# Optimization experiments

Measured on AMD Instinct MI355X. Metric: run time of the kernel, lower is better.

## Reference

```python
import jax, jax.numpy as jnp
import numpy as np

NI, NF = 100000, 2000
E, EF = 800000, 200000
DN, DE = 16, 8
NH, EH = 64, 8
NL = 11

def setup_inputs() -> dict:
    key = jax.random.key(0)
    ks = jax.random.split(key, 24)
    g = lambda k, shp, fan: jax.random.normal(k, shp, jnp.float32) / np.float32(np.sqrt(fan))
    inp = {
        'instruction_feats': jax.random.normal(ks[0], (NI, DN), jnp.float32),
        'final_feats': jax.random.normal(ks[1], (NF, DN), jnp.float32),
        'instruction_edge_feats': jax.random.normal(ks[2], (E, DE), jnp.float32),
        'to_final_edge_feats': jax.random.normal(ks[3], (EF, DE), jnp.float32),
        'prev_src': jax.random.randint(ks[4], (E,), 0, NI, jnp.int32),
        'prev_dst': jax.random.randint(ks[5], (E,), 0, NI, jnp.int32),
        'tf_src': jax.random.randint(ks[6], (EF,), 0, NI, jnp.int32),
        'tf_dst': jax.random.randint(ks[7], (EF,), 0, NF, jnp.int32),
        'W_it': g(ks[8], (DN, NH), DN), 'b_it': jnp.zeros((NH,), jnp.float32),
        'W_ft': g(ks[9], (DN, NH), DN), 'b_ft': jnp.zeros((NH,), jnp.float32),
        'W_ep': g(ks[10], (DE, EH), DE), 'b_ep': jnp.zeros((EH,), jnp.float32),
        'W_es': g(ks[11], (DE, EH), DE), 'b_es': jnp.zeros((EH,), jnp.float32),
        'W_ef': g(ks[12], (DE, EH), DE), 'b_ef': jnp.zeros((EH,), jnp.float32),
        'Wg_prev': g(ks[13], (NL, NH + EH, NH), NH + EH), 'bg_prev': jnp.zeros((NL, NH), jnp.float32),
        'Wg_succ': g(ks[14], (NL, NH + EH, NH), NH + EH), 'bg_succ': jnp.zeros((NL, NH), jnp.float32),
        'Wg_tf': g(ks[15], (NL, NH + EH, NH), NH + EH), 'bg_tf': jnp.zeros((NL, NH), jnp.float32),
        'Wr1': g(ks[16], (NH, NH), NH), 'br1': jnp.zeros((NH,), jnp.float32),
        'Wr2': g(ks[17], (NH, NH), NH), 'br2': jnp.zeros((NH,), jnp.float32),
        'Wr3': g(ks[18], (NH, 1), NH), 'br3': jnp.zeros((1,), jnp.float32),
    }
    return inp

def _mean_agg(src_feats, src_idx, dst_idx, edge_feats, W, b, n_dst):
    # gather-concat-dense per edge, then scatter-mean onto destinations
    msg = jnp.concatenate([src_feats[src_idx], edge_feats], axis=1) @ W + b  # [E, NH]
    s = jax.ops.segment_sum(msg, dst_idx, num_segments=n_dst)
    cnt = jax.ops.segment_sum(jnp.ones((msg.shape[0], 1), msg.dtype), dst_idx, num_segments=n_dst)
    return s / jnp.maximum(cnt, 1.0)  # zero-in-degree nodes get 0 (DGL mean semantics)

def reference(instruction_feats, final_feats, instruction_edge_feats, to_final_edge_feats,
              prev_src, prev_dst, tf_src, tf_dst,
              W_it, b_it, W_ft, b_ft, W_ep, b_ep, W_es, b_es, W_ef, b_ef,
              Wg_prev, bg_prev, Wg_succ, bg_succ, Wg_tf, bg_tf,
              Wr1, br1, Wr2, br2, Wr3, br3):
    elu = jax.nn.elu
    ni = instruction_feats.shape[0]
    nf = final_feats.shape[0]
    inst = elu(instruction_feats @ W_it + b_it)
    fin = elu(final_feats @ W_ft + b_ft)
    e_prev = elu(instruction_edge_feats @ W_ep + b_ep)
    e_succ = elu(instruction_edge_feats @ W_es + b_es)
    e_tf = elu(to_final_edge_feats @ W_ef + b_ef)
    succ_src, succ_dst = prev_dst, prev_src  # 'succ' is the reverse edge set
    for l in range(Wg_prev.shape[0]):
        o_p = _mean_agg(inst, prev_src, prev_dst, e_prev, Wg_prev[l], bg_prev[l], ni)
        o_s = _mean_agg(inst, succ_src, succ_dst, e_succ, Wg_succ[l], bg_succ[l], ni)
        o_f = _mean_agg(inst, tf_src, tf_dst, e_tf, Wg_tf[l], bg_tf[l], nf)
        inst = elu(inst + 0.5 * (o_p + o_s))
        fin = elu(fin + o_f)
    fin = elu(fin @ Wr1 + br1)
    fin = elu(fin @ Wr2 + br2)
    return jnp.squeeze(fin @ Wr3 + br3, axis=1)
```

## Files before the change

### kernel.cpp

```cpp
#include <hip/hip_runtime.h>
#include <math.h>

#define NI 100000
#define NF 2000
#define NE 800000
#define NEF 200000
#define DN 16
#define NL 11
#define NT (2 * NI + NF)
#define KX 160
#define NBI 782
#define NBF 125
#define WTN (64 * 168)

typedef short bf16x8 __attribute__((ext_vector_type(8)));
typedef float f32x4 __attribute__((ext_vector_type(4)));

__device__ __forceinline__ float elu1(float x) { return x > 0.f ? x : expm1f(x); }

__device__ __forceinline__ unsigned short f2bf(float f) {
    unsigned x = __float_as_uint(f);
    return (unsigned short)((x + 0x7fffu + ((x >> 16) & 1u)) >> 16);
}
__device__ __forceinline__ float bf2f(unsigned short u) {
    return __uint_as_float(((unsigned)u) << 16);
}

__global__ __launch_bounds__(256) void k_count(const int* __restrict__ prev_src,
                                               const int* __restrict__ prev_dst,
                                               const int* __restrict__ tf_dst,
                                               int* cnt) {
    int i = blockIdx.x * blockDim.x + threadIdx.x;
    if (i < NE) {
        atomicAdd(&cnt[prev_dst[i]], 1);
        atomicAdd(&cnt[NI + prev_src[i]], 1);
    }
    if (i < NEF) atomicAdd(&cnt[2 * NI + tf_dst[i]], 1);
}

__global__ __launch_bounds__(256) void k_scan1(const int* __restrict__ cnt, int n,
                                               int* __restrict__ rp, int* __restrict__ bsum) {
    __shared__ int s[256];
    int t = threadIdx.x, b = blockIdx.x, i = b * 256 + t;
    int v = (i < n) ? cnt[i] : 0;
    s[t] = v; __syncthreads();
    for (int o = 1; o < 256; o <<= 1) {
        int x = (t >= o) ? s[t - o] : 0;
        __syncthreads();
        s[t] += x;
        __syncthreads();
    }
    if (i < n) rp[i + 1] = s[t];
    if (t == 255) bsum[b] = s[255];
}

__global__ __launch_bounds__(1024) void k_scan2(int* __restrict__ bsum, int nb) {
    __shared__ int s[1024];
    int t = threadIdx.x;
    int v = (t < nb) ? bsum[t] : 0;
    s[t] = v; __syncthreads();
    for (int o = 1; o < 1024; o <<= 1) {
        int x = (t >= o) ? s[t - o] : 0;
        __syncthreads();
        s[t] += x;
        __syncthreads();
    }
    if (t < nb) bsum[t] = s[t] - v;
}

__global__ __launch_bounds__(256) void k_scan3(int* __restrict__ rp, const int* __restrict__ bsum, int n) {
    int i = blockIdx.x * blockDim.x + threadIdx.x;
    if (i < n) rp[i + 1] += bsum[i >> 8];
    if (i == 0) rp[0] = 0;
}

__global__ __launch_bounds__(256) void k_prep_w(const float* __restrict__ Wg_prev,
                                                const float* __restrict__ Wg_succ,
                                                unsigned short* __restrict__ wcat) {
    int idx = blockIdx.x * blockDim.x + threadIdx.x;
    if (idx >= NL * WTN) return;
    int l = idx / WTN;
    int r = idx - l * WTN;
    int n = r / 168, k = r - n * 168;
    float v = 0.f;
    if (k < 72)       v = 0.5f * Wg_prev[(size_t)l * 72 * 64 + k * 64 + n];
    else if (k < 144) v = 0.5f * Wg_succ[(size_t)l * 72 * 64 + (k - 72) * 64 + n];
    wcat[idx] = f2bf(v);
}

__global__ __launch_bounds__(256) void k_scatter(const int* __restrict__ prev_src,
                                                 const int* __restrict__ prev_dst,
                                                 const int* __restrict__ tf_src,
                                                 const int* __restrict__ tf_dst,
                                                 const float* __restrict__ xe,
                                                 const float* __restrict__ xef,
                                                 const int* __restrict__ rp,
                                                 int* fill,
                                                 int* colP, int* colS, int* colF,
                                                 float* __restrict__ ePbuf,
                                                 float* __restrict__ eSbuf,
                                                 float* __restrict__ eFbuf,
                                                 const float* __restrict__ Wep, const float* __restrict__ bep,
                                                 const float* __restrict__ Wes, const float* __restrict__ bes,
                                                 const float* __restrict__ Wef, const float* __restrict__ bef) {
    int i = blockIdx.x * blockDim.x + threadIdx.x;
    if (i < NE) {
        int s = prev_src[i], d = prev_dst[i];
        float4 x0 = ((const float4*)xe)[(size_t)i * 2];
        float4 x1 = ((const float4*)xe)[(size_t)i * 2 + 1];
        float x[8] = {x0.x, x0.y, x0.z, x0.w, x1.x, x1.y, x1.z, x1.w};
        float eP[8], eS[8];
#pragma unroll
        for (int j = 0; j < 8; j++) {
            float vp = bep[j], vs = bes[j];
#pragma unroll
            for (int k = 0; k < 8; k++) { vp += x[k] * Wep[k * 8 + j]; vs += x[k] * Wes[k * 8 + j]; }
            eP[j] = elu1(vp); eS[j] = elu1(vs);
        }
        int tP = rp[d] + atomicAdd(&fill[d], 1);
        colP[tP] = s;
        ((float4*)ePbuf)[(size_t)tP * 2]     = make_float4(eP[0], eP[1], eP[2], eP[3]);
        ((float4*)ePbuf)[(size_t)tP * 2 + 1] = make_float4(eP[4], eP[5], eP[6], eP[7]);
        int tS = rp[NI + s] - NE + atomicAdd(&fill[NI + s], 1);
        colS[tS] = d;
        ((float4*)eSbuf)[(size_t)tS * 2]     = make_float4(eS[0], eS[1], eS[2], eS[3]);
        ((float4*)eSbuf)[(size_t)tS * 2 + 1] = make_float4(eS[4], eS[5], eS[6], eS[7]);
    }
    if (i < NEF) {
        int s = tf_src[i], d = tf_dst[i];
        float4 x0 = ((const float4*)xef)[(size_t)i * 2];
        float4 x1 = ((const float4*)xef)[(size_t)i * 2 + 1];
        float x[8] = {x0.x, x0.y, x0.z, x0.w, x1.x, x1.y, x1.z, x1.w};
        float eF[8];
#pragma unroll
        for (int j = 0; j < 8; j++) {
            float v = bef[j];
#pragma unroll
            for (int k = 0; k < 8; k++) v += x[k] * Wef[k * 8 + j];
            eF[j] = elu1(v);
        }
        int tF = rp[2 * NI + d] - 2 * NE + atomicAdd(&fill[2 * NI + d], 1);
        colF[tF] = s;
        ((float4*)eFbuf)[(size_t)tF * 2]     = make_float4(eF[0], eF[1], eF[2], eF[3]);
        ((float4*)eFbuf)[(size_t)tF * 2 + 1] = make_float4(eF[4], eF[5], eF[6], eF[7]);
    }
}

__global__ __launch_bounds__(256) void k_eagg2(const int* __restrict__ rp,
                                               const float* __restrict__ ePbuf,
                                               const float* __restrict__ eSbuf,
                                               const float* __restrict__ eFbuf,
                                               float* __restrict__ aggEp,
                                               float* __restrict__ aggEs,
                                               float* __restrict__ aggEf) {
    int idx = blockIdx.x * blockDim.x + threadIdx.x;
    if (idx >= NT) return;
    const float* buf; float* out; int s, e;
    if (idx < NF) {
        int n = idx;
        s = rp[2 * NI + n] - 2 * NE; e = rp[2 * NI + n + 1] - 2 * NE;
        buf = eFbuf; out = aggEf + (size_t)n * 8;
    } else if (idx < NF + NI) {
        int n = idx - NF;
        s = rp[n]; e = rp[n + 1];
        buf = ePbuf; out = aggEp + (size_t)n * 8;
    } else {
        int n = idx - NF - NI;
        s = rp[NI + n] - NE; e = rp[NI + n + 1] - NE;
        buf = eSbuf; out = aggEs + (size_t)n * 8;
    }
    float a0 = 0.f, a1 = 0.f, a2 = 0.f, a3 = 0.f, a4 = 0.f, a5 = 0.f, a6 = 0.f, a7 = 0.f;
    for (int t = s; t < e; ++t) {
        float4 v0 = ((const float4*)buf)[(size_t)t * 2];
        float4 v1 = ((const float4*)buf)[(size_t)t * 2 + 1];
        a0 += v0.x; a1 += v0.y; a2 += v0.z; a3 += v0.w;
        a4 += v1.x; a5 += v1.y; a6 += v1.z; a7 += v1.w;
    }
    ((float4*)out)[0] = make_float4(a0, a1, a2, a3);
    ((float4*)out)[1] = make_float4(a4, a5, a6, a7);
}

__global__ __launch_bounds__(256) void k_prep_x(const int* __restrict__ rpAll,
                                                const float* __restrict__ aggEp,
                                                const float* __restrict__ aggEs,
                                                unsigned short* __restrict__ X) {
    int i = blockIdx.x * blockDim.x + threadIdx.x;
    if (i >= NI) return;
    int cP = rpAll[i + 1] - rpAll[i];
    int cS = rpAll[NI + i + 1] - rpAll[NI + i];
    float invP = 1.f / (float)max(cP, 1);
    float invS = 1.f / (float)max(cS, 1);
    unsigned short* xr = X + (size_t)i * KX;
#pragma unroll
    for (int c = 0; c < 2; c++) {
        float4 ep = ((const float4*)(aggEp + (size_t)i * 8))[c];
        float4 es = ((const float4*)(aggEs + (size_t)i * 8))[c];
        ushort4 up; up.x = f2bf(ep.x * invP); up.y = f2bf(ep.y * invP);
                    up.z = f2bf(ep.z * invP); up.w = f2bf(ep.w * invP);
        ushort4 us; us.x = f2bf(es.x * invS); us.y = f2bf(es.y * invS);
                    us.z = f2bf(es.z * invS); us.w = f2bf(es.w * invS);
        ((ushort4*)(xr + 64))[c]  = up;
        ((ushort4*)(xr + 136))[c] = us;
    }
    ushort4 z; z.x = z.y = z.z = z.w = 0;
#pragma unroll
    for (int c = 0; c < 4; c++) ((ushort4*)(xr + 144))[c] = z;
}

__global__ __launch_bounds__(256) void k_node_embed(const float* __restrict__ xi,
                                                    const float* __restrict__ xf,
                                                    const float* __restrict__ Wit, const float* __restrict__ bit,
                                                    const float* __restrict__ Wft, const float* __restrict__ bft,
                                                    float* __restrict__ inst, unsigned short* __restrict__ inst_bf,
                                                    float* __restrict__ fin) {
    const int NPW = 16;
    int lane = threadIdx.x & 63;
    int wave = (blockIdx.x * blockDim.x + threadIdx.x) >> 6;
    int base = wave * NPW;
    float wi[DN], wf[DN];
#pragma unroll
    for (int k = 0; k < DN; k++) { wi[k] = Wit[k * 64 + lane]; wf[k] = Wft[k * 64 + lane]; }
    float bi = bit[lane], bf = bft[lane];
    for (int n = 0; n < NPW; n++) {
        int i = base + n;
        if (i < NI) {
            const float4* x4 = (const float4*)(xi + (size_t)i * DN);
            float4 xa = x4[0], xb = x4[1], xc = x4[2], xd = x4[3];
            float x[DN] = {xa.x, xa.y, xa.z, xa.w, xb.x, xb.y, xb.z, xb.w,
                           xc.x, xc.y, xc.z, xc.w, xd.x, xd.y, xd.z, xd.w};
            float acc = bi;
#pragma unroll
            for (int k = 0; k < DN; k++) acc += x[k] * wi[k];
            float v = elu1(acc);
            inst[(size_t)i * 64 + lane] = v;
            inst_bf[(size_t)i * 64 + lane] = f2bf(v);
        } else if (i < NI + NF) {
            int f = i - NI;
            const float4* x4 = (const float4*)(xf + (size_t)f * DN);
            float4 xa = x4[0], xb = x4[1], xc = x4[2], xd = x4[3];
            float x[DN] = {xa.x, xa.y, xa.z, xa.w, xb.x, xb.y, xb.z, xb.w,
                           xc.x, xc.y, xc.z, xc.w, xd.x, xd.y, xd.z, xd.w};
            float acc = bf;
#pragma unroll
            for (int k = 0; k < DN; k++) acc += x[k] * wf[k];
            fin[(size_t)f * 64 + lane] = elu1(acc);
        }
    }
}

__global__ __launch_bounds__(256) void k_spmm(const unsigned short* __restrict__ inst_bf,
                                              const int* __restrict__ rp,
                                              const int* __restrict__ colP,
                                              const int* __restrict__ colS,
                                              const int* __restrict__ colF,
                                              unsigned short* __restrict__ X,
                                              float* __restrict__ aggHf) {
    int lane = threadIdx.x & 63;
    int wv = (blockIdx.x * blockDim.x + threadIdx.x) >> 6;
    int n3 = lane >> 3;
    int f8 = lane & 7;
    int task = wv * 8 + n3;
    if (task >= NT) return;

    const int* col; int i, rbase, ebase, xoff;
    if (task < NF)            { i = task;           rbase = 2 * NI; ebase = 2 * NE; col = colF; xoff = -1; }
    else if (task < NF + NI)  { i = task - NF;      rbase = 0;      ebase = 0;      col = colP; xoff = 0;  }
    else                      { i = task - NF - NI; rbase = NI;     ebase = NE;     col = colS; xoff = 72; }

    int s = rp[rbase + i] - ebase, e1 = rp[rbase + i + 1] - ebase;
    const unsigned short* src = inst_bf + f8 * 8;
    float a[8];
#pragma unroll
    for (int j = 0; j < 8; j++) a[j] = 0.f;

    int pos = s;
    for (; pos + 8 <= e1; pos += 8) {
        int c[8];
#pragma unroll
        for (int u = 0; u < 8; u++) c[u] = col[pos + u];
        bf16x8 v[8];
#pragma unroll
        for (int u = 0; u < 8; u++) v[u] = *(const bf16x8*)(src + (size_t)c[u] * 64);
#pragma unroll
        for (int u = 0; u < 8; u++) {
#pragma unroll
            for (int j = 0; j < 8; j++) a[j] += bf2f((unsigned short)v[u][j]);
        }
    }
    for (; pos + 4 <= e1; pos += 4) {
        int c0 = col[pos], c1 = col[pos + 1], c2 = col[pos + 2], c3 = col[pos + 3];
        bf16x8 v0 = *(const bf16x8*)(src + (size_t)c0 * 64);
        bf16x8 v1 = *(const bf16x8*)(src + (size_t)c1 * 64);
        bf16x8 v2 = *(const bf16x8*)(src + (size_t)c2 * 64);
        bf16x8 v3 = *(const bf16x8*)(src + (size_t)c3 * 64);
#pragma unroll
        for (int j = 0; j < 8; j++) a[j] += bf2f((unsigned short)v0[j]);
#pragma unroll
        for (int j = 0; j < 8; j++) a[j] += bf2f((unsigned short)v1[j]);
#pragma unroll
        for (int j = 0; j < 8; j++) a[j] += bf2f((unsigned short)v2[j]);
#pragma unroll
        for (int j = 0; j < 8; j++) a[j] += bf2f((unsigned short)v3[j]);
    }
    for (; pos < e1; ++pos) {
        int c = col[pos];
        bf16x8 v = *(const bf16x8*)(src + (size_t)c * 64);
#pragma unroll
        for (int j = 0; j < 8; j++) a[j] += bf2f((unsigned short)v[j]);
    }

    int cnt = e1 - s;
    float inv = cnt > 0 ? 1.f / (float)cnt : 0.f;
    if (xoff >= 0) {
        ushort4 o0, o1;
        o0.x = f2bf(a[0] * inv); o0.y = f2bf(a[1] * inv);
        o0.z = f2bf(a[2] * inv); o0.w = f2bf(a[3] * inv);
        o1.x = f2bf(a[4] * inv); o1.y = f2bf(a[5] * inv);
        o1.z = f2bf(a[6] * inv); o1.w = f2bf(a[7] * inv);
        unsigned short* dst = X + (size_t)i * KX + xoff + f8 * 8;
        *(ushort4*)dst = o0;
        *(ushort4*)(dst + 4) = o1;
    } else {
        float* dst = aggHf + (size_t)i * 64 + f8 * 8;
        *(float4*)dst = make_float4(a[0] * inv, a[1] * inv, a[2] * inv, a[3] * inv);
        *(float4*)(dst + 4) = make_float4(a[4] * inv, a[5] * inv, a[6] * inv, a[7] * inv);
    }
}

__global__ __launch_bounds__(256) void k_dense_layer(
    const unsigned short* __restrict__ X,
    float* __restrict__ inst, unsigned short* __restrict__ inst_bf,
    const int* __restrict__ rpAll,
    const unsigned short* __restrict__ wcat_l,
    const float* __restrict__ bp, const float* __restrict__ bs,
    float* __restrict__ fin,
    const float* __restrict__ aggHf, const float* __restrict__ aggEf,
    const float* __restrict__ Wf, const float* __restrict__ bf) {
    __shared__ __align__(16) unsigned short Wt[64][168];
    int t = threadIdx.x;

    if (blockIdx.x < NBI) {
        {
            const uint4* wsrc = (const uint4*)wcat_l;
            uint4* wdst = (uint4*)&Wt[0][0];
            for (int idx = t; idx < 1344; idx += 256) wdst[idx] = wsrc[idx];
        }
        __syncthreads();

        int wave = t >> 6, lane = t & 63;
        int rowbase = blockIdx.x * 128 + wave * 32;
        int lrow = lane & 15, lk = (lane >> 4) * 8;

        f32x4 acc[2][4];
#pragma unroll
        for (int rb = 0; rb < 2; rb++)
#pragma unroll
            for (int nb = 0; nb < 4; nb++) acc[rb][nb] = (f32x4){0.f, 0.f, 0.f, 0.f};

#pragma unroll
        for (int kc = 0; kc < 5; kc++) {
            int k0 = kc * 32 + lk;
            bf16x8 a[2], b[4];
#pragma unroll
            for (int rb = 0; rb < 2; rb++) {
                int r = min(rowbase + rb * 16 + lrow, NI - 1);
                a[rb] = *(const bf16x8*)(X + (size_t)r * KX + k0);
            }
#pragma unroll
            for (int nb = 0; nb < 4; nb++)
                b[nb] = *(const bf16x8*)(&Wt[nb * 16 + lrow][k0]);
#pragma unroll
            for (int rb = 0; rb < 2; rb++)
#pragma unroll
                for (int nb = 0; nb < 4; nb++)
                    acc[rb][nb] = __builtin_amdgcn_mfma_f32_16x16x32_bf16(a[rb], b[nb], acc[rb][nb], 0, 0, 0);
        }

#pragma unroll
        for (int rb = 0; rb < 2; rb++) {
#pragma unroll
            for (int j = 0; j < 4; j++) {
                int node = rowbase + rb * 16 + (lane >> 4) * 4 + j;
                bool v = node < NI;
                int nn = v ? node : NI - 1;
                float mP = (v && (rpAll[nn + 1] > rpAll[nn])) ? 0.5f : 0.f;
                float mS = (v && (rpAll[NI + nn + 1] > rpAll[NI + nn])) ? 0.5f : 0.f;
#pragma unroll
                for (int nb = 0; nb < 4; nb++) {
                    int col = nb * 16 + lrow;
                    float x = inst[(size_t)nn * 64 + col] + acc[rb][nb][j] + mP * bp[col] + mS * bs[col];
                    x = elu1(x);
                    if (v) {
                        inst[(size_t)nn * 64 + col] = x;
                        inst_bf[(size_t)nn * 64 + col] = f2bf(x);
                    }
                }
            }
        }
    } else {
        int tid = (blockIdx.x - NBI) * 256 + t;
        int n = tid >> 4;
        int jq = tid & 15;
        const int* rpF = rpAll + 2 * NI;
        int cF = rpF[n + 1] - rpF[n];
        float mF = (cF > 0) ? 1.f : 0.f;
        float invF = 1.f / (float)max(cF, 1);

        float acc0 = bf[jq * 4 + 0], acc1 = bf[jq * 4 + 1];
        float acc2 = bf[jq * 4 + 2], acc3 = bf[jq * 4 + 3];
        const float* hrow = aggHf + (size_t)n * 64;
        for (int k = 0; k < 64; k++) {
            float h = hrow[k];
            float4 w = *(const float4*)(Wf + (size_t)k * 64 + jq * 4);
            acc0 += h * w.x; acc1 += h * w.y; acc2 += h * w.z; acc3 += h * w.w;
        }
        const float* erow = aggEf + (size_t)n * 8;
#pragma unroll
        for (int k = 0; k < 8; k++) {
            float h = erow[k] * invF;
            float4 w = *(const float4*)(Wf + (size_t)(64 + k) * 64 + jq * 4);
            acc0 += h * w.x; acc1 += h * w.y; acc2 += h * w.z; acc3 += h * w.w;
        }
        float4 fv = *(const float4*)(fin + (size_t)n * 64 + jq * 4);
        float4 o;
        o.x = elu1(fv.x + mF * acc0);
        o.y = elu1(fv.y + mF * acc1);
        o.z = elu1(fv.z + mF * acc2);
        o.w = elu1(fv.w + mF * acc3);
        *(float4*)(fin + (size_t)n * 64 + jq * 4) = o;
    }
}

__global__ __launch_bounds__(64, 1) void k_head(
    const float* __restrict__ fin,
    const float* __restrict__ Wr1, const float* __restrict__ br1,
    const float* __restrict__ Wr2, const float* __restrict__ br2,
    const float* __restrict__ Wr3, const float* __restrict__ br3,
    float* __restrict__ out) {
    __shared__ float hL[64 * 65];
    const int lane = threadIdx.x;
    const int base = blockIdx.x * 64;

    for (int idx = lane; idx < 1024; idx += 64) {
        int n = idx >> 4, k4 = idx & 15;
        float4 v = ((const float4*)fin)[(size_t)min(base + n, NF - 1) * 16 + k4];
        float* d = &hL[n * 65 + k4 * 4];
        d[0] = v.x; d[1] = v.y; d[2] = v.z; d[3] = v.w;
    }
    __syncthreads();

    float acc[64];
#pragma unroll
    for (int j = 0; j < 64; j++) acc[j] = br1[j];
#pragma unroll 4
    for (int k = 0; k < 64; k++) {
        float h = hL[lane * 65 + k];
#pragma unroll
        for (int j = 0; j < 64; j++) acc[j] += h * Wr1[k * 64 + j];
    }
#pragma unroll
    for (int j = 0; j < 64; j++) hL[lane * 65 + j] = elu1(acc[j]);

#pragma unroll
    for (int j = 0; j < 64; j++) acc[j] = br2[j];
#pragma unroll 4
    for (int k = 0; k < 64; k++) {
        float h = hL[lane * 65 + k];
#pragma unroll
        for (int j = 0; j < 64; j++) acc[j] += h * Wr2[k * 64 + j];
    }
    float r = br3[0];
#pragma unroll
    for (int j = 0; j < 64; j++) r += elu1(acc[j]) * Wr3[j];

    int i = base + lane;
    if (i < NF) out[i] = r;
}

extern "C" void kernel_launch(void* const* d_in, const int* in_sizes, int n_in,
                              void* d_out, int out_size, void* d_ws, size_t ws_size,
                              hipStream_t stream) {
    const float* xi  = (const float*)d_in[0];
    const float* xf  = (const float*)d_in[1];
    const float* xe  = (const float*)d_in[2];
    const float* xef = (const float*)d_in[3];
    const int* prev_src = (const int*)d_in[4];
    const int* prev_dst = (const int*)d_in[5];
    const int* tf_src = (const int*)d_in[6];
    const int* tf_dst = (const int*)d_in[7];
    const float* W_it = (const float*)d_in[8];  const float* b_it = (const float*)d_in[9];
    const float* W_ft = (const float*)d_in[10]; const float* b_ft = (const float*)d_in[11];
    const float* W_ep = (const float*)d_in[12]; const float* b_ep = (const float*)d_in[13];
    const float* W_es = (const float*)d_in[14]; const float* b_es = (const float*)d_in[15];
    const float* W_ef = (const float*)d_in[16]; const float* b_ef = (const float*)d_in[17];
    const float* Wg_prev = (const float*)d_in[18]; const float* bg_prev = (const float*)d_in[19];
    const float* Wg_succ = (const float*)d_in[20]; const float* bg_succ = (const float*)d_in[21];
    const float* Wg_tf   = (const float*)d_in[22]; const float* bg_tf   = (const float*)d_in[23];
    const float* Wr1 = (const float*)d_in[24]; const float* br1 = (const float*)d_in[25];
    const float* Wr2 = (const float*)d_in[26]; const float* br2 = (const float*)d_in[27];
    const float* Wr3 = (const float*)d_in[28]; const float* br3 = (const float*)d_in[29];

    char* ws = (char*)d_ws;
    size_t off = 0;
    auto alloc = [&](size_t bytes) -> char* {
        char* p = ws + off;
        off += (bytes + 255) & ~(size_t)255;
        return p;
    };
    float* inst  = (float*)alloc((size_t)NI * 64 * 4);
    unsigned short* inst_bf = (unsigned short*)alloc((size_t)NI * 64 * 2);
    unsigned short* X = (unsigned short*)alloc((size_t)NI * KX * 2);
    float* fin   = (float*)alloc((size_t)NF * 64 * 4);
    float* aggHf = (float*)alloc((size_t)NF * 64 * 4);
    float* aggEp = (float*)alloc((size_t)NI * 8 * 4);
    float* aggEs = (float*)alloc((size_t)NI * 8 * 4);
    float* aggEf = (float*)alloc((size_t)NF * 8 * 4);
    unsigned short* wcat = (unsigned short*)alloc((size_t)NL * WTN * 2);
    char* zero_begin = ws + off;
    int* cnt  = (int*)alloc((size_t)NT * 4);
    int* fill = (int*)alloc((size_t)NT * 4);
    char* zero_end = ws + off;
    int* rpAll = (int*)alloc((size_t)(NT + 1) * 4);
    int* colP = (int*)alloc((size_t)NE * 4);
    int* colS = (int*)alloc((size_t)NE * 4);
    int* colF = (int*)alloc((size_t)NEF * 4);
    int* bsum = (int*)alloc(1024 * 4);
    (void)ws_size; (void)in_sizes; (void)n_in; (void)out_size;

    float* ePbuf = (float*)X;
    float* eSbuf = inst;
    float* eFbuf = (float*)inst_bf;

    hipMemsetAsync(zero_begin, 0, (size_t)(zero_end - zero_begin), stream);

    k_prep_w<<<(NL * WTN + 255) / 256, 256, 0, stream>>>(Wg_prev, Wg_succ, wcat);

    k_count<<<(NE + 255) / 256, 256, 0, stream>>>(prev_src, prev_dst, tf_dst, cnt);

    int nb = (NT + 255) / 256;
    k_scan1<<<nb, 256, 0, stream>>>(cnt, NT, rpAll, bsum);
    k_scan2<<<1, 1024, 0, stream>>>(bsum, nb);
    k_scan3<<<nb, 256, 0, stream>>>(rpAll, bsum, NT);

    k_scatter<<<(NE + 255) / 256, 256, 0, stream>>>(prev_src, prev_dst, tf_src, tf_dst,
                                                    xe, xef, rpAll, fill,
                                                    colP, colS, colF,
                                                    ePbuf, eSbuf, eFbuf,
                                                    W_ep, b_ep, W_es, b_es, W_ef, b_ef);

    k_eagg2<<<(NT + 255) / 256, 256, 0, stream>>>(rpAll, ePbuf, eSbuf, eFbuf,
                                                  aggEp, aggEs, aggEf);

    k_prep_x<<<(NI + 255) / 256, 256, 0, stream>>>(rpAll, aggEp, aggEs, X);

    {
        int waves = (NI + NF + 15) / 16;
        int blocks = (waves + 3) / 4;
        k_node_embed<<<blocks, 256, 0, stream>>>(xi, xf, W_it, b_it, W_ft, b_ft,
                                                 inst, inst_bf, fin);
    }

    for (int l = 0; l < NL; l++) {
        k_spmm<<<(NT + 31) / 32, 256, 0, stream>>>(inst_bf, rpAll,
                                                   colP, colS, colF,
                                                   X, aggHf);
        k_dense_layer<<<NBI + NBF, 256, 0, stream>>>(X, inst, inst_bf, rpAll,
                                                     wcat + (size_t)l * WTN,
                                                     bg_prev + (size_t)l * 64, bg_succ + (size_t)l * 64,
                                                     fin, aggHf, aggEf,
                                                     Wg_tf + (size_t)l * 72 * 64, bg_tf + (size_t)l * 64);
    }

    k_head<<<(NF + 63) / 64, 64, 0, stream>>>(fin, Wr1, br1, Wr2, br2, Wr3, br3, (float*)d_out);
}
```

Baseline: 1.058 ms.

## Fuse SpMM aggregation into dense layer kernel via shared-memory X tile

Merges the per-layer gather/mean-aggregation kernel and the dense MFMA layer into a single kernel. Each block gathers neighbour features for its 128 nodes straight into a shared-memory X tile, and the final-node blocks aggregate into shared memory, so the global X/aggHf round trip and one launch per layer go away. The inst_bf buffer is now ping-ponged to avoid read/write races across blocks, and the static edge-feature part of X is stored compactly. Weights are now read from global memory instead of being staged in LDS. The gather phase now runs inside the GEMM blocks, which may lower parallelism and occupancy.

```diff
diff --git a/kernel.cpp b/kernel.cpp
--- a/kernel.cpp
+++ b/kernel.cpp
@@ -8,10 +8,10 @@
 #define DN 16
 #define NL 11
 #define NT (2 * NI + NF)
-#define KX 160
 #define NBI 782
 #define NBF 125
 #define WTN (64 * 168)
+#define LROW 168
 
 typedef short bf16x8 __attribute__((ext_vector_type(8)));
 typedef float f32x4 __attribute__((ext_vector_type(4)));
@@ -183,14 +183,14 @@
 __global__ __launch_bounds__(256) void k_prep_x(const int* __restrict__ rpAll,
                                                 const float* __restrict__ aggEp,
                                                 const float* __restrict__ aggEs,
-                                                unsigned short* __restrict__ X) {
+                                                unsigned short* __restrict__ Xme) {
     int i = blockIdx.x * blockDim.x + threadIdx.x;
     if (i >= NI) return;
     int cP = rpAll[i + 1] - rpAll[i];
     int cS = rpAll[NI + i + 1] - rpAll[NI + i];
     float invP = 1.f / (float)max(cP, 1);
     float invS = 1.f / (float)max(cS, 1);
-    unsigned short* xr = X + (size_t)i * KX;
+    unsigned short* xr = Xme + (size_t)i * 16;
 #pragma unroll
     for (int c = 0; c < 2; c++) {
         float4 ep = ((const float4*)(aggEp + (size_t)i * 8))[c];
@@ -199,12 +199,9 @@
                     up.z = f2bf(ep.z * invP); up.w = f2bf(ep.w * invP);
         ushort4 us; us.x = f2bf(es.x * invS); us.y = f2bf(es.y * invS);
                     us.z = f2bf(es.z * invS); us.w = f2bf(es.w * invS);
-        ((ushort4*)(xr + 64))[c]  = up;
-        ((ushort4*)(xr + 136))[c] = us;
-    }
-    ushort4 z; z.x = z.y = z.z = z.w = 0;
-#pragma unroll
-    for (int c = 0; c < 4; c++) ((ushort4*)(xr + 144))[c] = z;
+        ((ushort4*)xr)[c]     = up;
+        ((ushort4*)xr)[2 + c] = us;
+    }
 }
 
 __global__ __launch_bounds__(256) void k_node_embed(const float* __restrict__ xi,
@@ -248,31 +245,11 @@
     }
 }
 
-__global__ __launch_bounds__(256) void k_spmm(const unsigned short* __restrict__ inst_bf,
-                                              const int* __restrict__ rp,
-                                              const int* __restrict__ colP,
-                                              const int* __restrict__ colS,
-                                              const int* __restrict__ colF,
-                                              unsigned short* __restrict__ X,
-                                              float* __restrict__ aggHf) {
-    int lane = threadIdx.x & 63;
-    int wv = (blockIdx.x * blockDim.x + threadIdx.x) >> 6;
-    int n3 = lane >> 3;
-    int f8 = lane & 7;
-    int task = wv * 8 + n3;
-    if (task >= NT) return;
-
-    const int* col; int i, rbase, ebase, xoff;
-    if (task < NF)            { i = task;           rbase = 2 * NI; ebase = 2 * NE; col = colF; xoff = -1; }
-    else if (task < NF + NI)  { i = task - NF;      rbase = 0;      ebase = 0;      col = colP; xoff = 0;  }
-    else                      { i = task - NF - NI; rbase = NI;     ebase = NE;     col = colS; xoff = 72; }
-
-    int s = rp[rbase + i] - ebase, e1 = rp[rbase + i + 1] - ebase;
-    const unsigned short* src = inst_bf + f8 * 8;
-    float a[8];
+__device__ __forceinline__ void spmm_chain(const unsigned short* __restrict__ src,
+                                           const int* __restrict__ col,
+                                           int s, int e1, float* a) {
 #pragma unroll
     for (int j = 0; j < 8; j++) a[j] = 0.f;
-
     int pos = s;
     for (; pos + 8 <= e1; pos += 8) {
         int c[8];
@@ -308,48 +285,71 @@
 #pragma unroll
         for (int j = 0; j < 8; j++) a[j] += bf2f((unsigned short)v[j]);
     }
-
-    int cnt = e1 - s;
-    float inv = cnt > 0 ? 1.f / (float)cnt : 0.f;
-    if (xoff >= 0) {
-        ushort4 o0, o1;
-        o0.x = f2bf(a[0] * inv); o0.y = f2bf(a[1] * inv);
-        o0.z = f2bf(a[2] * inv); o0.w = f2bf(a[3] * inv);
-        o1.x = f2bf(a[4] * inv); o1.y = f2bf(a[5] * inv);
-        o1.z = f2bf(a[6] * inv); o1.w = f2bf(a[7] * inv);
-        unsigned short* dst = X + (size_t)i * KX + xoff + f8 * 8;
-        *(ushort4*)dst = o0;
-        *(ushort4*)(dst + 4) = o1;
-    } else {
-        float* dst = aggHf + (size_t)i * 64 + f8 * 8;
-        *(float4*)dst = make_float4(a[0] * inv, a[1] * inv, a[2] * inv, a[3] * inv);
-        *(float4*)(dst + 4) = make_float4(a[4] * inv, a[5] * inv, a[6] * inv, a[7] * inv);
-    }
-}
-
-__global__ __launch_bounds__(256) void k_dense_layer(
-    const unsigned short* __restrict__ X,
-    float* __restrict__ inst, unsigned short* __restrict__ inst_bf,
-    const int* __restrict__ rpAll,
+}
+
+__global__ __launch_bounds__(256) void k_layer(
+    const unsigned short* __restrict__ inst_bf_in,
+    const int* __restrict__ rp,
+    const int* __restrict__ colP, const int* __restrict__ colS, const int* __restrict__ colF,
+    const unsigned short* __restrict__ Xme,
+    float* __restrict__ inst, unsigned short* __restrict__ inst_bf_out,
     const unsigned short* __restrict__ wcat_l,
     const float* __restrict__ bp, const float* __restrict__ bs,
     float* __restrict__ fin,
-    const float* __restrict__ aggHf, const float* __restrict__ aggEf,
+    const float* __restrict__ aggEf,
     const float* __restrict__ Wf, const float* __restrict__ bf) {
-    __shared__ __align__(16) unsigned short Wt[64][168];
+    __shared__ __align__(16) unsigned short sh[128 * LROW];
     int t = threadIdx.x;
+    int wave = t >> 6, lane = t & 63;
+    int n3 = lane >> 3, f8 = lane & 7;
 
     if (blockIdx.x < NBI) {
+        int rowbase = blockIdx.x * 128;
         {
-            const uint4* wsrc = (const uint4*)wcat_l;
-            uint4* wdst = (uint4*)&Wt[0][0];
-            for (int idx = t; idx < 1344; idx += 256) wdst[idx] = wsrc[idx];
+            int row = t >> 1, sel = t & 1;
+            int node = min(rowbase + row, NI - 1);
+            const unsigned short* xm = Xme + (size_t)node * 16;
+            unsigned short* xr = sh + row * LROW;
+            ushort4 z4; z4.x = z4.y = z4.z = z4.w = 0;
+            if (sel == 0) {
+                *(ushort4*)(xr + 64) = *(const ushort4*)(xm);
+                *(ushort4*)(xr + 68) = *(const ushort4*)(xm + 4);
+                *(ushort4*)(xr + 144) = z4;
+                *(ushort4*)(xr + 148) = z4;
+            } else {
+                *(ushort4*)(xr + 136) = *(const ushort4*)(xm + 8);
+                *(ushort4*)(xr + 140) = *(const ushort4*)(xm + 12);
+                *(ushort4*)(xr + 152) = z4;
+                *(ushort4*)(xr + 156) = z4;
+            }
+        }
+        const unsigned short* src = inst_bf_in + f8 * 8;
+        for (int rep = 0; rep < 8; rep++) {
+            int tl = rep * 32 + wave * 8 + n3;
+            int node_local = tl >> 1, dir = tl & 1;
+            int node = rowbase + node_local;
+            if (node < NI) {
+                const int* col = dir ? colS : colP;
+                int rb_ = dir ? NI : 0, eb = dir ? NE : 0, xoff = dir ? 72 : 0;
+                int s = rp[rb_ + node] - eb, e1 = rp[rb_ + node + 1] - eb;
+                float a[8];
+                spmm_chain(src, col, s, e1, a);
+                int cnt = e1 - s;
+                float inv = cnt > 0 ? 1.f / (float)cnt : 0.f;
+                ushort4 o0, o1;
+                o0.x = f2bf(a[0] * inv); o0.y = f2bf(a[1] * inv);
+                o0.z = f2bf(a[2] * inv); o0.w = f2bf(a[3] * inv);
+                o1.x = f2bf(a[4] * inv); o1.y = f2bf(a[5] * inv);
+                o1.z = f2bf(a[6] * inv); o1.w = f2bf(a[7] * inv);
+                unsigned short* dst = sh + node_local * LROW + xoff + f8 * 8;
+                *(ushort4*)dst = o0;
+                *(ushort4*)(dst + 4) = o1;
+            }
         }
         __syncthreads();
 
-        int wave = t >> 6, lane = t & 63;
-        int rowbase = blockIdx.x * 128 + wave * 32;
         int lrow = lane & 15, lk = (lane >> 4) * 8;
+        int wrow = wave * 32;
 
         f32x4 acc[2][4];
 #pragma unroll
@@ -362,13 +362,11 @@
             int k0 = kc * 32 + lk;
             bf16x8 a[2], b[4];
 #pragma unroll
-            for (int rb = 0; rb < 2; rb++) {
-                int r = min(rowbase + rb * 16 + lrow, NI - 1);
-                a[rb] = *(const bf16x8*)(X + (size_t)r * KX + k0);
-            }
+            for (int rb = 0; rb < 2; rb++)
+                a[rb] = *(const bf16x8*)(sh + (wrow + rb * 16 + lrow) * LROW + k0);
 #pragma unroll
             for (int nb = 0; nb < 4; nb++)
-                b[nb] = *(const bf16x8*)(&Wt[nb * 16 + lrow][k0]);
+                b[nb] = *(const bf16x8*)(wcat_l + (size_t)(nb * 16 + lrow) * 168 + k0);
 #pragma unroll
             for (int rb = 0; rb < 2; rb++)
 #pragma unroll
@@ -380,11 +378,11 @@
         for (int rb = 0; rb < 2; rb++) {
 #pragma unroll
             for (int j = 0; j < 4; j++) {
-                int node = rowbase + rb * 16 + (lane >> 4) * 4 + j;
+                int node = rowbase + wrow + rb * 16 + (lane >> 4) * 4 + j;
                 bool v = node < NI;
                 int nn = v ? node : NI - 1;
-                float mP = (v && (rpAll[nn + 1] > rpAll[nn])) ? 0.5f : 0.f;
-                float mS = (v && (rpAll[NI + nn + 1] > rpAll[NI + nn])) ? 0.5f : 0.f;
+                float mP = (v && (rp[nn + 1] > rp[nn])) ? 0.5f : 0.f;
+                float mS = (v && (rp[NI + nn + 1] > rp[NI + nn])) ? 0.5f : 0.f;
 #pragma unroll
                 for (int nb = 0; nb < 4; nb++) {
                     int col = nb * 16 + lrow;
@@ -392,23 +390,40 @@
                     x = elu1(x);
                     if (v) {
                         inst[(size_t)nn * 64 + col] = x;
-                        inst_bf[(size_t)nn * 64 + col] = f2bf(x);
+                        inst_bf_out[(size_t)nn * 64 + col] = f2bf(x);
                     }
                 }
             }
         }
     } else {
-        int tid = (blockIdx.x - NBI) * 256 + t;
-        int n = tid >> 4;
-        int jq = tid & 15;
-        const int* rpF = rpAll + 2 * NI;
+        int nbase = (blockIdx.x - NBI) * 16;
+        float* aggH = (float*)sh;
+        if (wave < 2) {
+            int nl = wave * 8 + n3;
+            int node = nbase + nl;
+            const unsigned short* src = inst_bf_in + f8 * 8;
+            int s = rp[2 * NI + node] - 2 * NE, e1 = rp[2 * NI + node + 1] - 2 * NE;
+            float a[8];
+            spmm_chain(src, colF, s, e1, a);
+            int cnt = e1 - s;
+            float inv = cnt > 0 ? 1.f / (float)cnt : 0.f;
+            float* dst = aggH + nl * 64 + f8 * 8;
+            *(float4*)dst = make_float4(a[0] * inv, a[1] * inv, a[2] * inv, a[3] * inv);
+            *(float4*)(dst + 4) = make_float4(a[4] * inv, a[5] * inv, a[6] * inv, a[7] * inv);
+        }
+        __syncthreads();
+
+        int n4 = t >> 4;
+        int jq = t & 15;
+        int n = nbase + n4;
+        const int* rpF = rp + 2 * NI;
         int cF = rpF[n + 1] - rpF[n];
         float mF = (cF > 0) ? 1.f : 0.f;
         float invF = 1.f / (float)max(cF, 1);
 
         float acc0 = bf[jq * 4 + 0], acc1 = bf[jq * 4 + 1];
         float acc2 = bf[jq * 4 + 2], acc3 = bf[jq * 4 + 3];
-        const float* hrow = aggHf + (size_t)n * 64;
+        const float* hrow = aggH + n4 * 64;
         for (int k = 0; k < 64; k++) {
             float h = hrow[k];
             float4 w = *(const float4*)(Wf + (size_t)k * 64 + jq * 4);
@@ -508,10 +523,11 @@
         return p;
     };
     float* inst  = (float*)alloc((size_t)NI * 64 * 4);
-    unsigned short* inst_bf = (unsigned short*)alloc((size_t)NI * 64 * 2);
-    unsigned short* X = (unsigned short*)alloc((size_t)NI * KX * 2);
+    unsigned short* inst_bfA = (unsigned short*)alloc((size_t)NI * 64 * 2);
+    unsigned short* inst_bfB = (unsigned short*)alloc((size_t)NI * 64 * 2);
+    float* ePbuf = (float*)alloc((size_t)NE * 8 * 4);
+    unsigned short* Xme = (unsigned short*)alloc((size_t)NI * 16 * 2);
     float* fin   = (float*)alloc((size_t)NF * 64 * 4);
-    float* aggHf = (float*)alloc((size_t)NF * 64 * 4);
     float* aggEp = (float*)alloc((size_t)NI * 8 * 4);
     float* aggEs = (float*)alloc((size_t)NI * 8 * 4);
     float* aggEf = (float*)alloc((size_t)NF * 8 * 4);
@@ -527,9 +543,8 @@
     int* bsum = (int*)alloc(1024 * 4);
     (void)ws_size; (void)in_sizes; (void)n_in; (void)out_size;
 
-    float* ePbuf = (float*)X;
     float* eSbuf = inst;
-    float* eFbuf = (float*)inst_bf;
+    float* eFbuf = (float*)inst_bfA;
 
     hipMemsetAsync(zero_begin, 0, (size_t)(zero_end - zero_begin), stream);
 
@@ -551,24 +566,24 @@
     k_eagg2<<<(NT + 255) / 256, 256, 0, stream>>>(rpAll, ePbuf, eSbuf, eFbuf,
                                                   aggEp, aggEs, aggEf);
 
-    k_prep_x<<<(NI + 255) / 256, 256, 0, stream>>>(rpAll, aggEp, aggEs, X);
+    k_prep_x<<<(NI + 255) / 256, 256, 0, stream>>>(rpAll, aggEp, aggEs, Xme);
 
     {
         int waves = (NI + NF + 15) / 16;
         int blocks = (waves + 3) / 4;
         k_node_embed<<<blocks, 256, 0, stream>>>(xi, xf, W_it, b_it, W_ft, b_ft,
-                                                 inst, inst_bf, fin);
-    }
-
+                                                 inst, inst_bfA, fin);
+    }
+
+    unsigned short* bufs[2] = {inst_bfA, inst_bfB};
     for (int l = 0; l < NL; l++) {
-        k_spmm<<<(NT + 31) / 32, 256, 0, stream>>>(inst_bf, rpAll,
-                                                   colP, colS, colF,
-                                                   X, aggHf);
-        k_dense_layer<<<NBI + NBF, 256, 0, stream>>>(X, inst, inst_bf, rpAll,
-                                                     wcat + (size_t)l * WTN,
-                                                     bg_prev + (size_t)l * 64, bg_succ + (size_t)l * 64,
-                                                     fin, aggHf, aggEf,
-                                                     Wg_tf + (size_t)l * 72 * 64, bg_tf + (size_t)l * 64);
+        k_layer<<<NBI + NBF, 256, 0, stream>>>(bufs[l & 1], rpAll,
+                                               colP, colS, colF, Xme,
+                                               inst, bufs[(l + 1) & 1],
+                                               wcat + (size_t)l * WTN,
+                                               bg_prev + (size_t)l * 64, bg_succ + (size_t)l * 64,
+                                               fin, aggEf,
+                                               Wg_tf + (size_t)l * 72 * 64, bg_tf + (size_t)l * 64);
     }
 
     k_head<<<(NF + 63) / 64, 64, 0, stream>>>(fin, Wr1, br1, Wr2, br2, Wr3, br3, (float*)d_out);
```

Measured after the change: 2.324 ms. 2.2x slower.
